# Performance work log

Measured on AMD Instinct MI355X. Metric: run time of the kernel, lower is better.

## Reference

```python
import jax, jax.numpy as jnp
import numpy as np

USER_NUM = 128          # K: users, also equals RIS elements N due to W_v packing
NOISE_DBM = -80.0       # downlink_noise_power
N0 = 10.0 ** (NOISE_DBM / 10.0) / 1000.0  # = exp(p/10*ln10)/1000


def setup_inputs() -> dict:
    key = jax.random.key(0)
    k1, k2, k3, k4, k5 = jax.random.split(key, 5)
    M, K, N = 1024, USER_NUM, USER_NUM  # antennas, users, RIS elements
    return {
        "W_v": jax.random.normal(k1, (M + 1, 2 * K), dtype=jnp.float32),
        "A_real": jax.random.normal(k2, (K, M, N), dtype=jnp.float32),
        "A_imag": jax.random.normal(k3, (K, M, N), dtype=jnp.float32),
        "h_d_real": jax.random.normal(k4, (K, M), dtype=jnp.float32),
        "h_d_imag": jax.random.normal(k5, (K, M), dtype=jnp.float32),
    }


def reference(W_v, A_real, A_imag, h_d_real, h_d_imag):
    # unpack: row 0 is v (RIS phase vector), rows 1.. are W (beamformers)
    v = W_v[0]            # [2N]
    W = W_v[1:]           # [M, 2K]
    C = W.shape[1] // 2   # = K = user_num = N
    W_re, W_im = W[:, :C], W[:, C:]      # [M, K]
    v_re, v_im = v[:C], v[C:]            # [N]

    # effective channel h_k = h_d[k] + A[k] @ v  (complex product, real arithmetic)
    Av_re = jnp.einsum('kmn,n->km', A_real, v_re) - jnp.einsum('kmn,n->km', A_imag, v_im)
    Av_im = jnp.einsum('kmn,n->km', A_imag, v_re) + jnp.einsum('kmn,n->km', A_real, v_im)
    h_re = h_d_real + Av_re              # [K, M]
    h_im = h_d_imag + Av_im              # [K, M]

    # gamma[k, i] = w_i^T h_k (complex, no conjugate, matching the block-matrix math)
    g_re = h_re @ W_re - h_im @ W_im     # [K, K]
    g_im = h_re @ W_im + h_im @ W_re     # [K, K]
    mag = jnp.sqrt(g_re * g_re + g_im * g_im)  # |gamma| (modulus, NOT squared)

    sig = jnp.diagonal(mag)                       # |w_k^T h_k|
    interf = jnp.sum(mag, axis=1) - sig           # sum_{i != k} |w_i^T h_k|
    R = sig / (interf + N0)                       # per-user 'rate' term
    return (-jnp.sum(R) * 1.0e6)[None]            # shape (1,), matches torch.zeros(1) accumulator
```

## Files before the change

kernel.cpp:

```cpp
#include <hip/hip_runtime.h>


#define KM_ROWS (128 * 1024)

typedef float vf4 __attribute__((ext_vector_type(4)));

__device__ __forceinline__ float dot4v(vf4 a, const float4& b) {
    return a.x*b.x + a.y*b.y + a.z*b.z + a.w*b.w;
}

template<int CTRL>
__device__ __forceinline__ float dpp_xadd(float x) {
    union { float f; int i; } u, v;
    u.f = x;
    v.i = __builtin_amdgcn_mov_dpp(u.i, CTRL, 0xf, 0xf, false);
    return x + v.f;
}

__device__ __forceinline__ float sum16(float x) {
    x = dpp_xadd<0xB1>(x);
    x = dpp_xadd<0x4E>(x);
    x = dpp_xadd<0x141>(x);
    x = dpp_xadd<0x140>(x);
    return x;
}

__global__ __launch_bounds__(256) void compute_h_kernel(
    const float* __restrict__ A_real,
    const float* __restrict__ A_imag,
    const float* __restrict__ W_v,
    const float* __restrict__ h_d_real,
    const float* __restrict__ h_d_imag,
    float* __restrict__ h_re,
    float* __restrict__ h_im)
{
    const int lane = threadIdx.x & 63;
    const int sub  = lane & 15;
    const int rsub = lane >> 4;
    const int base = blockIdx.x * 4 + (threadIdx.x >> 6);

    const float4 vr0 = ((const float4*)W_v)[sub];
    const float4 vr1 = ((const float4*)W_v)[sub + 16];
    const float4 vi0 = ((const float4*)W_v)[32 + sub];
    const float4 vi1 = ((const float4*)W_v)[48 + sub];

    const int r0 = base * 8 + rsub;
    const int r1 = r0 + 4;
    const vf4* Ar0 = (const vf4*)(A_real + (size_t)r0 * 128);
    const vf4* Ai0 = (const vf4*)(A_imag + (size_t)r0 * 128);
    const vf4* Ar1 = (const vf4*)(A_real + (size_t)r1 * 128);
    const vf4* Ai1 = (const vf4*)(A_imag + (size_t)r1 * 128);

    const vf4 a0 = __builtin_nontemporal_load(Ar0 + sub);
    const vf4 a1 = __builtin_nontemporal_load(Ar0 + sub + 16);
    const vf4 b0 = __builtin_nontemporal_load(Ai0 + sub);
    const vf4 b1 = __builtin_nontemporal_load(Ai0 + sub + 16);
    const vf4 c0 = __builtin_nontemporal_load(Ar1 + sub);
    const vf4 c1 = __builtin_nontemporal_load(Ar1 + sub + 16);
    const vf4 d0 = __builtin_nontemporal_load(Ai1 + sub);
    const vf4 d1 = __builtin_nontemporal_load(Ai1 + sub + 16);

    const float hdr0 = h_d_real[r0], hdi0 = h_d_imag[r0];
    const float hdr1 = h_d_real[r1], hdi1 = h_d_imag[r1];

    float p_re = dot4v(a0, vr0) + dot4v(a1, vr1) - dot4v(b0, vi0) - dot4v(b1, vi1);
    float p_im = dot4v(b0, vr0) + dot4v(b1, vr1) + dot4v(a0, vi0) + dot4v(a1, vi1);
    float q_re = dot4v(c0, vr0) + dot4v(c1, vr1) - dot4v(d0, vi0) - dot4v(d1, vi1);
    float q_im = dot4v(d0, vr0) + dot4v(d1, vr1) + dot4v(c0, vi0) + dot4v(c1, vi1);

    p_re = sum16(p_re);
    p_im = sum16(p_im);
    q_re = sum16(q_re);
    q_im = sum16(q_im);

    if (sub == 0) {
        h_re[r0] = hdr0 + p_re;
        h_im[r0] = hdi0 + p_im;
        h_re[r1] = hdr1 + q_re;
        h_im[r1] = hdi1 + q_im;
    }
}

__global__ __launch_bounds__(256) void gemm_partial_kernel(
    const float* __restrict__ h_re,
    const float* __restrict__ h_im,
    const float* __restrict__ W_v,
    float* __restrict__ part_re,
    float* __restrict__ part_im,
    float* __restrict__ out)
{
    const int kp    = blockIdx.x >> 3;
    const int slice = blockIdx.x & 7;
    const int t  = threadIdx.x;
    const int c4 = t & 31;
    const int seg = t >> 5;

    if (blockIdx.x == 0 && t == 0) *out = 0.f;

    const int k0 = kp, k1 = kp + 64;

    __shared__ float sh_re[2][128], sh_im[2][128];
    if (t < 128) {
        sh_re[0][t] = h_re[k0 * 1024 + slice * 128 + t];
        sh_im[0][t] = h_im[k0 * 1024 + slice * 128 + t];
    } else {
        sh_re[1][t - 128] = h_re[k1 * 1024 + slice * 128 + (t - 128)];
        sh_im[1][t - 128] = h_im[k1 * 1024 + slice * 128 + (t - 128)];
    }
    __syncthreads();

    const float* Wb = W_v + 256 + (size_t)(slice * 128) * 256;
    float4 gre0 = {0,0,0,0}, gim0 = {0,0,0,0};
    float4 gre1 = {0,0,0,0}, gim1 = {0,0,0,0};
    const int m0 = seg * 16;
    #pragma unroll 4
    for (int m = m0; m < m0 + 16; ++m) {
        const float4* Wr4 = (const float4*)(Wb + m * 256);
        float4 wr = Wr4[c4];
        float4 wi = Wr4[c4 + 32];
        float hr0 = sh_re[0][m], hi0 = sh_im[0][m];
        float hr1 = sh_re[1][m], hi1 = sh_im[1][m];
        gre0.x = fmaf(hr0, wr.x, fmaf(-hi0, wi.x, gre0.x));
        gre0.y = fmaf(hr0, wr.y, fmaf(-hi0, wi.y, gre0.y));
        gre0.z = fmaf(hr0, wr.z, fmaf(-hi0, wi.z, gre0.z));
        gre0.w = fmaf(hr0, wr.w, fmaf(-hi0, wi.w, gre0.w));
        gim0.x = fmaf(hr0, wi.x, fmaf(hi0, wr.x, gim0.x));
        gim0.y = fmaf(hr0, wi.y, fmaf(hi0, wr.y, gim0.y));
        gim0.z = fmaf(hr0, wi.z, fmaf(hi0, wr.z, gim0.z));
        gim0.w = fmaf(hr0, wi.w, fmaf(hi0, wr.w, gim0.w));
        gre1.x = fmaf(hr1, wr.x, fmaf(-hi1, wi.x, gre1.x));
        gre1.y = fmaf(hr1, wr.y, fmaf(-hi1, wi.y, gre1.y));
        gre1.z = fmaf(hr1, wr.z, fmaf(-hi1, wi.z, gre1.z));
        gre1.w = fmaf(hr1, wr.w, fmaf(-hi1, wi.w, gre1.w));
        gim1.x = fmaf(hr1, wi.x, fmaf(hi1, wr.x, gim1.x));
        gim1.y = fmaf(hr1, wi.y, fmaf(hi1, wr.y, gim1.y));
        gim1.z = fmaf(hr1, wi.z, fmaf(hi1, wr.z, gim1.z));
        gim1.w = fmaf(hr1, wi.w, fmaf(hi1, wr.w, gim1.w));
    }

    __shared__ float4 s_re[2][256], s_im[2][256];
    s_re[0][t] = gre0; s_im[0][t] = gim0;
    s_re[1][t] = gre1; s_im[1][t] = gim1;
    __syncthreads();
    if (t < 64) {
        const int u  = t >> 5;
        const int cg = t & 31;
        float4 r = s_re[u][cg], i = s_im[u][cg];
        #pragma unroll
        for (int s = 1; s < 8; ++s) {
            float4 rr = s_re[u][s * 32 + cg], ii = s_im[u][s * 32 + cg];
            r.x += rr.x; r.y += rr.y; r.z += rr.z; r.w += rr.w;
            i.x += ii.x; i.y += ii.y; i.z += ii.z; i.w += ii.w;
        }
        const int k = (u == 0) ? k0 : k1;
        float4* pr = (float4*)(part_re + (size_t)(slice * 128 + k) * 128);
        float4* pi = (float4*)(part_im + (size_t)(slice * 128 + k) * 128);
        pr[cg] = r;
        pi[cg] = i;
    }
}

__global__ __launch_bounds__(128) void rate_kernel(
    const float* __restrict__ part_re,
    const float* __restrict__ part_im,
    float* __restrict__ out)
{
    const int k = blockIdx.x;
    const int c = threadIdx.x;

    float gr = 0.f, gi = 0.f;
    #pragma unroll
    for (int s = 0; s < 8; ++s) {
        gr += part_re[(s * 128 + k) * 128 + c];
        gi += part_im[(s * 128 + k) * 128 + c];
    }
    float mag = sqrtf(gr * gr + gi * gi);

    __shared__ float s_sig;
    __shared__ float s_w[2];
    if (c == k) s_sig = mag;

    float v = mag;
    #pragma unroll
    for (int off = 32; off > 0; off >>= 1) v += __shfl_xor(v, off);
    if ((c & 63) == 0) s_w[c >> 6] = v;
    __syncthreads();

    if (c == 0) {
        float total  = s_w[0] + s_w[1];
        float interf = total - s_sig;
        float R      = s_sig / (interf + 1e-11f);
        atomicAdd(out, -R * 1e6f);
    }
}

extern "C" void kernel_launch(void* const* d_in, const int* in_sizes, int n_in,
                              void* d_out, int out_size, void* d_ws, size_t ws_size,
                              hipStream_t stream) {
    const float* W_v      = (const float*)d_in[0];
    const float* A_real   = (const float*)d_in[1];
    const float* A_imag   = (const float*)d_in[2];
    const float* h_d_real = (const float*)d_in[3];
    const float* h_d_imag = (const float*)d_in[4];
    float* out  = (float*)d_out;

    float* h_re    = (float*)d_ws;
    float* h_im    = h_re + KM_ROWS;
    float* part_re = h_im + KM_ROWS;
    float* part_im = part_re + 8 * 128 * 128;

    compute_h_kernel<<<4096, 256, 0, stream>>>(A_real, A_imag, W_v,
                                               h_d_real, h_d_imag, h_re, h_im);
    gemm_partial_kernel<<<512, 256, 0, stream>>>(h_re, h_im, W_v,
                                                 part_re, part_im, out);
    rate_kernel<<<128, 128, 0, stream>>>(part_re, part_im, out);
}
```

Baseline: 158.0 us.

## Fuse effective-channel computation into the gamma GEMM, keeping h in shared memory

Merges the A·v reduction kernel and the partial GEMM kernel into a single kernel. Each block now computes the h values for its two users and a 64-row M slice, stores them in shared memory and uses them directly in the partial GEMM. The M dimension is split into 16 slices instead of 8, so the rate kernel sums 16 partials. This removes the global round-trip for h and one launch. In exchange each block does more serial work, and the 1024-block grid gives fewer, heavier blocks for streaming the 128 MB of A.

```diff
diff --git a/kernel.cpp b/kernel.cpp
--- a/kernel.cpp
+++ b/kernel.cpp
@@ -1,7 +1,8 @@
 #include <hip/hip_runtime.h>
 
 
-#define KM_ROWS (128 * 1024)
+#define NSLICE 16
+#define MSL    64
 
 typedef float vf4 __attribute__((ext_vector_type(4)));
 
@@ -25,96 +26,80 @@
     return x;
 }
 
-__global__ __launch_bounds__(256) void compute_h_kernel(
+__global__ __launch_bounds__(256, 4) void fused_hg_kernel(
     const float* __restrict__ A_real,
     const float* __restrict__ A_imag,
     const float* __restrict__ W_v,
     const float* __restrict__ h_d_real,
     const float* __restrict__ h_d_imag,
-    float* __restrict__ h_re,
-    float* __restrict__ h_im)
+    float* __restrict__ part_re,
+    float* __restrict__ part_im,
+    float* __restrict__ out)
 {
-    const int lane = threadIdx.x & 63;
-    const int sub  = lane & 15;
-    const int rsub = lane >> 4;
-    const int base = blockIdx.x * 4 + (threadIdx.x >> 6);
+    const int kp    = blockIdx.x >> 4;
+    const int slice = blockIdx.x & 15;
+    const int t     = threadIdx.x;
+    const int lane  = t & 63;
+    const int wv    = t >> 6;
+    const int sub   = lane & 15;
+    const int rsub  = lane >> 4;
+    const int k0 = kp, k1 = kp + 64;
+
+    if (blockIdx.x == 0 && t == 0) *out = 0.f;
+
+    __shared__ float sh_re[2][MSL], sh_im[2][MSL];
 
     const float4 vr0 = ((const float4*)W_v)[sub];
     const float4 vr1 = ((const float4*)W_v)[sub + 16];
     const float4 vi0 = ((const float4*)W_v)[32 + sub];
     const float4 vi1 = ((const float4*)W_v)[48 + sub];
 
-    const int r0 = base * 8 + rsub;
-    const int r1 = r0 + 4;
-    const vf4* Ar0 = (const vf4*)(A_real + (size_t)r0 * 128);
-    const vf4* Ai0 = (const vf4*)(A_imag + (size_t)r0 * 128);
-    const vf4* Ar1 = (const vf4*)(A_real + (size_t)r1 * 128);
-    const vf4* Ai1 = (const vf4*)(A_imag + (size_t)r1 * 128);
+    #pragma unroll
+    for (int it = 0; it < 4; ++it) {
+        const int row = (wv * 4 + it) * 8 + rsub;
+        const int u   = row >> 6;
+        const int ml  = row & 63;
+        const int k   = u ? k1 : k0;
+        const size_t rb = (size_t)k * 1024 + (size_t)slice * MSL + ml;
+        const vf4* Ar0 = (const vf4*)(A_real + rb * 128);
+        const vf4* Ai0 = (const vf4*)(A_imag + rb * 128);
 
-    const vf4 a0 = __builtin_nontemporal_load(Ar0 + sub);
-    const vf4 a1 = __builtin_nontemporal_load(Ar0 + sub + 16);
-    const vf4 b0 = __builtin_nontemporal_load(Ai0 + sub);
-    const vf4 b1 = __builtin_nontemporal_load(Ai0 + sub + 16);
-    const vf4 c0 = __builtin_nontemporal_load(Ar1 + sub);
-    const vf4 c1 = __builtin_nontemporal_load(Ar1 + sub + 16);
-    const vf4 d0 = __builtin_nontemporal_load(Ai1 + sub);
-    const vf4 d1 = __builtin_nontemporal_load(Ai1 + sub + 16);
+        const vf4 a0 = __builtin_nontemporal_load(Ar0 + sub);
+        const vf4 a1 = __builtin_nontemporal_load(Ar0 + sub + 16);
+        const vf4 b0 = __builtin_nontemporal_load(Ai0 + sub);
+        const vf4 b1 = __builtin_nontemporal_load(Ai0 + sub + 16);
+        const vf4 c0 = __builtin_nontemporal_load(Ar0 + 128 + sub);
+        const vf4 c1 = __builtin_nontemporal_load(Ar0 + 128 + sub + 16);
+        const vf4 d0 = __builtin_nontemporal_load(Ai0 + 128 + sub);
+        const vf4 d1 = __builtin_nontemporal_load(Ai0 + 128 + sub + 16);
 
-    const float hdr0 = h_d_real[r0], hdi0 = h_d_imag[r0];
-    const float hdr1 = h_d_real[r1], hdi1 = h_d_imag[r1];
+        float p_re = dot4v(a0, vr0) + dot4v(a1, vr1) - dot4v(b0, vi0) - dot4v(b1, vi1);
+        float p_im = dot4v(b0, vr0) + dot4v(b1, vr1) + dot4v(a0, vi0) + dot4v(a1, vi1);
+        float q_re = dot4v(c0, vr0) + dot4v(c1, vr1) - dot4v(d0, vi0) - dot4v(d1, vi1);
+        float q_im = dot4v(d0, vr0) + dot4v(d1, vr1) + dot4v(c0, vi0) + dot4v(c1, vi1);
 
-    float p_re = dot4v(a0, vr0) + dot4v(a1, vr1) - dot4v(b0, vi0) - dot4v(b1, vi1);
-    float p_im = dot4v(b0, vr0) + dot4v(b1, vr1) + dot4v(a0, vi0) + dot4v(a1, vi1);
-    float q_re = dot4v(c0, vr0) + dot4v(c1, vr1) - dot4v(d0, vi0) - dot4v(d1, vi1);
-    float q_im = dot4v(d0, vr0) + dot4v(d1, vr1) + dot4v(c0, vi0) + dot4v(c1, vi1);
+        p_re = sum16(p_re);
+        p_im = sum16(p_im);
+        q_re = sum16(q_re);
+        q_im = sum16(q_im);
 
-    p_re = sum16(p_re);
-    p_im = sum16(p_im);
-    q_re = sum16(q_re);
-    q_im = sum16(q_im);
-
-    if (sub == 0) {
-        h_re[r0] = hdr0 + p_re;
-        h_im[r0] = hdi0 + p_im;
-        h_re[r1] = hdr1 + q_re;
-        h_im[r1] = hdi1 + q_im;
-    }
-}
-
-__global__ __launch_bounds__(256) void gemm_partial_kernel(
-    const float* __restrict__ h_re,
-    const float* __restrict__ h_im,
-    const float* __restrict__ W_v,
-    float* __restrict__ part_re,
-    float* __restrict__ part_im,
-    float* __restrict__ out)
-{
-    const int kp    = blockIdx.x >> 3;
-    const int slice = blockIdx.x & 7;
-    const int t  = threadIdx.x;
-    const int c4 = t & 31;
-    const int seg = t >> 5;
-
-    if (blockIdx.x == 0 && t == 0) *out = 0.f;
-
-    const int k0 = kp, k1 = kp + 64;
-
-    __shared__ float sh_re[2][128], sh_im[2][128];
-    if (t < 128) {
-        sh_re[0][t] = h_re[k0 * 1024 + slice * 128 + t];
-        sh_im[0][t] = h_im[k0 * 1024 + slice * 128 + t];
-    } else {
-        sh_re[1][t - 128] = h_re[k1 * 1024 + slice * 128 + (t - 128)];
-        sh_im[1][t - 128] = h_im[k1 * 1024 + slice * 128 + (t - 128)];
+        if (sub == 0) {
+            sh_re[u][ml]     = h_d_real[rb]     + p_re;
+            sh_im[u][ml]     = h_d_imag[rb]     + p_im;
+            sh_re[u][ml + 4] = h_d_real[rb + 4] + q_re;
+            sh_im[u][ml + 4] = h_d_imag[rb + 4] + q_im;
+        }
     }
     __syncthreads();
 
-    const float* Wb = W_v + 256 + (size_t)(slice * 128) * 256;
+    const int c4  = t & 31;
+    const int seg = t >> 5;
+    const float* Wb = W_v + 256 + (size_t)(slice * MSL) * 256;
     float4 gre0 = {0,0,0,0}, gim0 = {0,0,0,0};
     float4 gre1 = {0,0,0,0}, gim1 = {0,0,0,0};
-    const int m0 = seg * 16;
-    #pragma unroll 4
-    for (int m = m0; m < m0 + 16; ++m) {
+    const int m0 = seg * 8;
+    #pragma unroll
+    for (int m = m0; m < m0 + 8; ++m) {
         const float4* Wr4 = (const float4*)(Wb + m * 256);
         float4 wr = Wr4[c4];
         float4 wi = Wr4[c4 + 32];
@@ -170,7 +155,7 @@
 
     float gr = 0.f, gi = 0.f;
     #pragma unroll
-    for (int s = 0; s < 8; ++s) {
+    for (int s = 0; s < NSLICE; ++s) {
         gr += part_re[(s * 128 + k) * 128 + c];
         gi += part_im[(s * 128 + k) * 128 + c];
     }
@@ -204,14 +189,11 @@
     const float* h_d_imag = (const float*)d_in[4];
     float* out  = (float*)d_out;
 
-    float* h_re    = (float*)d_ws;
-    float* h_im    = h_re + KM_ROWS;
-    float* part_re = h_im + KM_ROWS;
-    float* part_im = part_re + 8 * 128 * 128;
+    float* part_re = (float*)d_ws;
+    float* part_im = part_re + NSLICE * 128 * 128;
 
-    compute_h_kernel<<<4096, 256, 0, stream>>>(A_real, A_imag, W_v,
-                                               h_d_real, h_d_imag, h_re, h_im);
-    gemm_partial_kernel<<<512, 256, 0, stream>>>(h_re, h_im, W_v,
-                                                 part_re, part_im, out);
+    fused_hg_kernel<<<1024, 256, 0, stream>>>(A_real, A_imag, W_v,
+                                              h_d_real, h_d_imag,
+                                              part_re, part_im, out);
     rate_kernel<<<128, 128, 0, stream>>>(part_re, part_im, out);
 }
```

Measured after the change: 154.0 us. -2.5%, faster.
